# Performance work log

Hardware: AMD Instinct MI355X
Metric: run time of the kernel (lower is better)

Reference implementation:

```python
import jax, jax.numpy as jnp
import numpy as np

E, I, O = 8, 1024, 1024   # num_experts, in_features, out_features
B = 16                    # number of molecular systems (segments)
N = 16384                 # total rows (atoms * coeffs); sum(mole_sizes) == N


def setup_inputs() -> dict:
    key = jax.random.key(0)
    k1, k2, k3, k4 = jax.random.split(key, 4)
    scale = (1.0 / I) ** 0.5
    x = jax.random.normal(k1, (N, I), dtype=jnp.float32)
    # init_linear: uniform(-k, k) with k = sqrt(1/in_features)
    weights = scale * 2.0 * (jax.random.uniform(k2, (E, O, I), dtype=jnp.float32) - 0.5)
    bias = scale * 2.0 * (jax.random.uniform(k3, (O,), dtype=jnp.float32) - 0.5)
    expert_mixing_coefficients = jax.random.uniform(k4, (B, E), dtype=jnp.float32)
    # segment sizes per system; equal sizes summing exactly to N (static under jit)
    mole_sizes = jnp.full((B,), N // B, dtype=jnp.int32)
    return {
        "x": x,
        "weights": weights,
        "bias": bias,
        "expert_mixing_coefficients": expert_mixing_coefficients,
        "mole_sizes": mole_sizes,
    }


def reference(x, weights, bias, expert_mixing_coefficients, mole_sizes):
    # Original: W_b = einsum('eoi,be->bio', weights, coeff); then segment_mm
    # applies x_seg_b @ W_b for each row-segment b.  By linearity this equals
    # projecting x through each expert and mixing with per-row coefficients,
    # which avoids materializing [B, I, O] synthesized weights per segment
    # while computing identical math.
    n = x.shape[0]
    b = expert_mixing_coefficients.shape[0]
    seg_id = jnp.repeat(jnp.arange(b), mole_sizes, total_repeat_length=n)  # [N]
    ct = expert_mixing_coefficients[seg_id]                               # [N, E]
    proj = jnp.einsum('ni,eoi->neo', x, weights)                          # [N, E, O]
    y = jnp.einsum('neo,ne->no', proj, ct) + bias                         # [N, O]
    return y
```

## Files before the change

### kernel.cpp

```cpp
#include <hip/hip_runtime.h>
#include <hip/hip_bf16.h>
#include <stdint.h>

constexpr int E_NUM  = 8;
constexpr int I_DIM  = 1024;
constexpr int O_DIM  = 1024;
constexpr int B_SEG  = 16;
constexpr int N_ROWS = 16384;

constexpr int BM = 256, BN = 256, BK = 64;
constexpr int NT = I_DIM / BK;

typedef __bf16 bf16x8 __attribute__((ext_vector_type(8)));
typedef float  f32x4  __attribute__((ext_vector_type(4)));
typedef unsigned short ushortx4 __attribute__((ext_vector_type(4)));

#define AS1 __attribute__((address_space(1)))
#define AS3 __attribute__((address_space(3)))

__device__ __forceinline__ unsigned short f2bf(float f) {
    unsigned int u = __float_as_uint(f);
    u += 0x7fffu + ((u >> 16) & 1u);
    return (unsigned short)(u >> 16);
}

__global__ __launch_bounds__(256) void prep(const float* __restrict__ x,
                                            unsigned short* __restrict__ xb,
                                            const float* __restrict__ w,
                                            const float* __restrict__ coeff,
                                            unsigned short* __restrict__ wb) {
    __shared__ float sc[B_SEG * E_NUM];
    const int bid = blockIdx.x;
    const int tid = threadIdx.x;
    const int q  = bid / 5;
    const int r5 = bid % 5;

    if (r5 == 0) {
        if (tid < B_SEG * E_NUM) sc[tid] = coeff[tid];
        __syncthreads();

        const size_t idx = ((size_t)q * 256 + tid) * 4;
        float4 wv[E_NUM];
#pragma unroll
        for (int e = 0; e < E_NUM; e++)
            wv[e] = *(const float4*)(w + (size_t)e * O_DIM * I_DIM + idx);

#pragma unroll
        for (int b = 0; b < B_SEG; b++) {
            float a0 = 0.f, a1 = 0.f, a2 = 0.f, a3 = 0.f;
#pragma unroll
            for (int e = 0; e < E_NUM; e++) {
                const float c = sc[b * E_NUM + e];
                a0 += c * wv[e].x; a1 += c * wv[e].y;
                a2 += c * wv[e].z; a3 += c * wv[e].w;
            }
            ushortx4 o;
            o[0] = f2bf(a0); o[1] = f2bf(a1); o[2] = f2bf(a2); o[3] = f2bf(a3);
            *(ushortx4*)(wb + (size_t)b * O_DIM * I_DIM + idx) = o;
        }
    } else {
        const int cidx = q * 4 + (r5 - 1);
        const size_t base = (size_t)cidx * 4096;
#pragma unroll
        for (int k = 0; k < 4; k++) {
            const size_t i = base + (size_t)(k * 256 + tid) * 4;
            const float4 v = *(const float4*)(x + i);
            ushortx4 o;
            o[0] = f2bf(v.x); o[1] = f2bf(v.y); o[2] = f2bf(v.z); o[3] = f2bf(v.w);
            *(ushortx4*)(xb + i) = o;
        }
    }
}

__device__ __forceinline__ bf16x8 lds_read_b128(unsigned addr) {
    bf16x8 r;
    asm volatile("ds_read_b128 %0, %1" : "=v"(r) : "v"(addr));
    return r;
}

__global__ __launch_bounds__(512, 2) void gemm_moe(
    const unsigned short* __restrict__ xb,
    const unsigned short* __restrict__ wb,
    const float* __restrict__ bias,
    const int* __restrict__ msz,
    float* __restrict__ out)
{
    __shared__ __align__(16) char sLDS[131072];

    const int lid  = blockIdx.x;
    const int xcd  = lid & 7;
    const int idx  = lid >> 3;
    const int seg  = (xcd << 1) | (idx >> 4);
    const int t16  = idx & 15;
    const int mblk = t16 >> 2;
    const int nblk = t16 & 3;

    int off = 0;
    for (int b = 0; b < seg; b++) off += msz[b];
    const int row0 = off + mblk * BM;
    const int col0 = nblk * BN;
    const unsigned short* wseg = wb + (size_t)seg * O_DIM * I_DIM;

    const int tid  = threadIdx.x;
    const int wave = tid >> 6;
    const int lane = tid & 63;
    const int wr = wave >> 2, wc = wave & 3;
    const int quad = lane >> 4, l16 = lane & 15;

    const int srow8  = lane >> 3;
    const int schunk = (lane & 7) ^ srow8;
    const unsigned short* gA0 = xb   + (size_t)(row0 + wave * 8 + srow8) * I_DIM + schunk * 8;
    const unsigned short* gA1 = gA0 + (size_t)128 * I_DIM;
    const unsigned short* gB0 = wseg + (size_t)(col0 + wave * 8 + srow8) * I_DIM + schunk * 8;
    const unsigned short* gB1 = gB0 + (size_t)128 * I_DIM;

    const unsigned rdA0 = (unsigned)((wr * 16 + l16) * 128 + (((0 + quad) ^ (l16 & 7)) * 16));
    const unsigned rdA1 = (unsigned)((wr * 16 + l16) * 128 + (((4 + quad) ^ (l16 & 7)) * 16));
    const unsigned rdB0 = (unsigned)(65536 + (wc * 16 + l16) * 128 + (((0 + quad) ^ (l16 & 7)) * 16));
    const unsigned rdB1 = (unsigned)(65536 + (wc * 16 + l16) * 128 + (((4 + quad) ^ (l16 & 7)) * 16));

    bf16x8 af0[4][2], af1[4][2], b0[2][2], b1[2][2];
    f32x4 acc[8][4];
#pragma unroll
    for (int m = 0; m < 8; ++m)
#pragma unroll
        for (int n = 0; n < 4; ++n)
            acc[m][n] = (f32x4){0.f, 0.f, 0.f, 0.f};

#define LOAD_A(DST, S) do { _Pragma("unroll") for (int mm = 0; mm < 4; ++mm) {      \
        DST[mm][0] = lds_read_b128(rdA0 + (S) * 16384u + mm * 4096u);               \
        DST[mm][1] = lds_read_b128(rdA1 + (S) * 16384u + mm * 4096u); } } while (0)
#define LOAD_B(DST, S) do { _Pragma("unroll") for (int nn = 0; nn < 2; ++nn) {      \
        DST[nn][0] = lds_read_b128(rdB0 + (S) * 16384u + nn * 8192u);               \
        DST[nn][1] = lds_read_b128(rdB1 + (S) * 16384u + nn * 8192u); } } while (0)

#define STAGE_A(H, S, ST) do {                                                      \
        const unsigned short* g_ = ((H) ? gA1 : gA0) + (size_t)(ST) * 64;           \
        __builtin_amdgcn_global_load_lds((const AS1 void*)g_,                       \
            (AS3 void*)(sLDS + (S) * 16384 + wave * 1024), 16, 0, 0);               \
        __builtin_amdgcn_global_load_lds((const AS1 void*)(g_ + (size_t)64 * I_DIM),\
            (AS3 void*)(sLDS + (S) * 16384 + 8192 + wave * 1024), 16, 0, 0); } while (0)
#define STAGE_B(H, S, ST) do {                                                      \
        const unsigned short* g_ = ((H) ? gB1 : gB0) + (size_t)(ST) * 64;           \
        __builtin_amdgcn_global_load_lds((const AS1 void*)g_,                       \
            (AS3 void*)(sLDS + 65536 + (S) * 16384 + wave * 1024), 16, 0, 0);       \
        __builtin_amdgcn_global_load_lds((const AS1 void*)(g_ + (size_t)64 * I_DIM),\
            (AS3 void*)(sLDS + 65536 + (S) * 16384 + 8192 + wave * 1024), 16, 0, 0); } while (0)

#define MFMA_Q(MH, NH, A, BV) do { _Pragma("unroll") for (int mm = 0; mm < 4; ++mm) \
        _Pragma("unroll") for (int nn = 0; nn < 2; ++nn)                            \
        _Pragma("unroll") for (int kk = 0; kk < 2; ++kk)                            \
            acc[(MH) * 4 + mm][(NH) * 2 + nn] =                                     \
                __builtin_amdgcn_mfma_f32_16x16x32_bf16(A[mm][kk], BV[nn][kk],      \
                    acc[(MH) * 4 + mm][(NH) * 2 + nn], 0, 0, 0); } while (0)

#define PH_MID() do { __builtin_amdgcn_sched_barrier(0);                            \
        __builtin_amdgcn_s_barrier();                                               \
        asm volatile("s_waitcnt lgkmcnt(0)");                                       \
        __builtin_amdgcn_sched_barrier(0);                                          \
        __builtin_amdgcn_s_setprio(1); } while (0)
#define PH_END_W() do { __builtin_amdgcn_s_setprio(0);                              \
        __builtin_amdgcn_sched_barrier(0);                                          \
        asm volatile("s_waitcnt vmcnt(4)");                                         \
        __builtin_amdgcn_sched_barrier(0);                                          \
        __builtin_amdgcn_s_barrier(); } while (0)
#define PH_END_N() do { __builtin_amdgcn_s_setprio(0);                              \
        __builtin_amdgcn_sched_barrier(0);                                          \
        __builtin_amdgcn_s_barrier(); } while (0)

#define TILE(R0, R1, S0, S1, ST) do {                                               \
        LOAD_A(af0, R0); LOAD_B(b0, R0); STAGE_A(0, S0, ST);                        \
        PH_MID(); MFMA_Q(0, 0, af0, b0); PH_END_W();                                \
        LOAD_A(af1, R1); STAGE_B(0, S0, ST);                                        \
        PH_MID(); MFMA_Q(1, 0, af1, b0); PH_END_W();                                \
        LOAD_B(b1, R1); STAGE_A(1, S1, ST);                                         \
        PH_MID(); MFMA_Q(1, 1, af1, b1); PH_END_N();                                \
        STAGE_B(1, S1, ST);                                                         \
        PH_MID(); MFMA_Q(0, 1, af0, b1); PH_END_W();                                \
    } while (0)

    STAGE_A(0, 0, 0); STAGE_B(0, 0, 0);
    STAGE_A(1, 1, 0); STAGE_B(1, 1, 0);
    asm volatile("s_waitcnt vmcnt(4)");
    __builtin_amdgcn_sched_barrier(0);
    __builtin_amdgcn_s_barrier();

#pragma unroll 1
    for (int tp = 0; tp < 8; ++tp) {
        const int t0 = 2 * tp, t1 = t0 + 1;
        const int st0 = (t0 + 1 < NT) ? t0 + 1 : NT - 1;
        const int st1 = (t1 + 1 < NT) ? t1 + 1 : NT - 1;
        TILE(0, 1, 2, 3, st0);
        TILE(2, 3, 0, 1, st1);
    }

#undef TILE
#undef PH_END_N
#undef PH_END_W
#undef PH_MID
#undef MFMA_Q
#undef STAGE_B
#undef STAGE_A
#undef LOAD_B
#undef LOAD_A

    float bv[4];
#pragma unroll
    for (int n = 0; n < 4; ++n)
        bv[n] = bias[col0 + n * 64 + wc * 16 + l16];

#pragma unroll
    for (int m = 0; m < 8; ++m) {
#pragma unroll
        for (int r = 0; r < 4; ++r) {
            int row = row0 + m * 32 + wr * 16 + quad * 4 + r;
            float* po = out + (size_t)row * O_DIM + col0 + wc * 16 + l16;
#pragma unroll
            for (int n = 0; n < 4; ++n)
                po[n * 64] = acc[m][n][r] + bv[n];
        }
    }
}

extern "C" void kernel_launch(void* const* d_in, const int* in_sizes, int n_in,
                              void* d_out, int out_size, void* d_ws, size_t ws_size,
                              hipStream_t stream) {
    const float* x     = (const float*)d_in[0];
    const float* w     = (const float*)d_in[1];
    const float* bias  = (const float*)d_in[2];
    const float* coeff = (const float*)d_in[3];
    const int*   msz   = (const int*)d_in[4];
    float* out = (float*)d_out;

    unsigned short* xb = (unsigned short*)d_ws;
    unsigned short* wb = xb + (size_t)N_ROWS * I_DIM;

    prep<<<5120, 256, 0, stream>>>(x, xb, w, coeff, wb);

    gemm_moe<<<B_SEG * (1024 / BM) * (1024 / BN), 512, 0, stream>>>(xb, wb, bias, msz, out);
}
```

Baseline: 195.4 us.

## Fuse x fp32-to-bf16 conversion into GEMM A-tile staging via registers

Drops the separate pass that converted x to bf16 in the prep kernel. The GEMM now loads fp32 x rows into registers, packs them to bf16 with v_cvt_pk_bf16_f32, and writes them swizzled into LDS inside the pipelined tile loop. The prep kernel now only synthesizes the mixed weights, with each thread handling two vectors. This removes the 64MB fp32 read plus 32MB bf16 write and read round trip for x. In exchange each GEMM tile reads x at twice the bytes, uses more registers, and adds LDS write traffic and tighter wait scheduling. Within the 4x4 tile grid of each segment, the four N-blocks sharing an M-block each load and convert the same x rows.

Measured after the change: 203.2 us. 4.0% more time.

```diff
diff --git a/kernel.cpp b/kernel.cpp
--- a/kernel.cpp
+++ b/kernel.cpp
@@ -14,6 +14,7 @@
 typedef __bf16 bf16x8 __attribute__((ext_vector_type(8)));
 typedef float  f32x4  __attribute__((ext_vector_type(4)));
 typedef unsigned short ushortx4 __attribute__((ext_vector_type(4)));
+typedef unsigned int   u32x4    __attribute__((ext_vector_type(4)));
 
 #define AS1 __attribute__((address_space(1)))
 #define AS3 __attribute__((address_space(3)))
@@ -24,51 +25,40 @@
     return (unsigned short)(u >> 16);
 }
 
-__global__ __launch_bounds__(256) void prep(const float* __restrict__ x,
-                                            unsigned short* __restrict__ xb,
-                                            const float* __restrict__ w,
+__global__ __launch_bounds__(256) void prep(const float* __restrict__ w,
                                             const float* __restrict__ coeff,
                                             unsigned short* __restrict__ wb) {
     __shared__ float sc[B_SEG * E_NUM];
-    const int bid = blockIdx.x;
     const int tid = threadIdx.x;
-    const int q  = bid / 5;
-    const int r5 = bid % 5;
-
-    if (r5 == 0) {
-        if (tid < B_SEG * E_NUM) sc[tid] = coeff[tid];
-        __syncthreads();
-
-        const size_t idx = ((size_t)q * 256 + tid) * 4;
-        float4 wv[E_NUM];
-#pragma unroll
-        for (int e = 0; e < E_NUM; e++)
-            wv[e] = *(const float4*)(w + (size_t)e * O_DIM * I_DIM + idx);
-
-#pragma unroll
-        for (int b = 0; b < B_SEG; b++) {
-            float a0 = 0.f, a1 = 0.f, a2 = 0.f, a3 = 0.f;
-#pragma unroll
-            for (int e = 0; e < E_NUM; e++) {
-                const float c = sc[b * E_NUM + e];
-                a0 += c * wv[e].x; a1 += c * wv[e].y;
-                a2 += c * wv[e].z; a3 += c * wv[e].w;
-            }
-            ushortx4 o;
-            o[0] = f2bf(a0); o[1] = f2bf(a1); o[2] = f2bf(a2); o[3] = f2bf(a3);
-            *(ushortx4*)(wb + (size_t)b * O_DIM * I_DIM + idx) = o;
+    if (tid < B_SEG * E_NUM) sc[tid] = coeff[tid];
+    __syncthreads();
+
+    const size_t s0 = (size_t)blockIdx.x * 512 + tid;
+    const size_t s1 = s0 + 256;
+    float4 wv0[E_NUM], wv1[E_NUM];
+#pragma unroll
+    for (int e = 0; e < E_NUM; e++) {
+        wv0[e] = *(const float4*)(w + (size_t)e * O_DIM * I_DIM + s0 * 4);
+        wv1[e] = *(const float4*)(w + (size_t)e * O_DIM * I_DIM + s1 * 4);
+    }
+
+#pragma unroll
+    for (int b = 0; b < B_SEG; b++) {
+        float a0 = 0.f, a1 = 0.f, a2 = 0.f, a3 = 0.f;
+        float c0 = 0.f, c1 = 0.f, c2 = 0.f, c3 = 0.f;
+#pragma unroll
+        for (int e = 0; e < E_NUM; e++) {
+            const float c = sc[b * E_NUM + e];
+            a0 += c * wv0[e].x; a1 += c * wv0[e].y;
+            a2 += c * wv0[e].z; a3 += c * wv0[e].w;
+            c0 += c * wv1[e].x; c1 += c * wv1[e].y;
+            c2 += c * wv1[e].z; c3 += c * wv1[e].w;
         }
-    } else {
-        const int cidx = q * 4 + (r5 - 1);
-        const size_t base = (size_t)cidx * 4096;
-#pragma unroll
-        for (int k = 0; k < 4; k++) {
-            const size_t i = base + (size_t)(k * 256 + tid) * 4;
-            const float4 v = *(const float4*)(x + i);
-            ushortx4 o;
-            o[0] = f2bf(v.x); o[1] = f2bf(v.y); o[2] = f2bf(v.z); o[3] = f2bf(v.w);
-            *(ushortx4*)(xb + i) = o;
-        }
+        ushortx4 o0, o1;
+        o0[0] = f2bf(a0); o0[1] = f2bf(a1); o0[2] = f2bf(a2); o0[3] = f2bf(a3);
+        o1[0] = f2bf(c0); o1[1] = f2bf(c1); o1[2] = f2bf(c2); o1[3] = f2bf(c3);
+        *(ushortx4*)(wb + (size_t)b * O_DIM * I_DIM + s0 * 4) = o0;
+        *(ushortx4*)(wb + (size_t)b * O_DIM * I_DIM + s1 * 4) = o1;
     }
 }
 
@@ -77,9 +67,17 @@
     asm volatile("ds_read_b128 %0, %1" : "=v"(r) : "v"(addr));
     return r;
 }
+__device__ __forceinline__ void lds_write_b128(unsigned addr, u32x4 v) {
+    asm volatile("ds_write_b128 %0, %1" :: "v"(addr), "v"(v) : "memory");
+}
+__device__ __forceinline__ unsigned cvt_pk_bf16(float lo, float hi) {
+    unsigned r;
+    asm("v_cvt_pk_bf16_f32 %0, %1, %2" : "=v"(r) : "v"(lo), "v"(hi));
+    return r;
+}
 
 __global__ __launch_bounds__(512, 2) void gemm_moe(
-    const unsigned short* __restrict__ xb,
+    const float* __restrict__ x,
     const unsigned short* __restrict__ wb,
     const float* __restrict__ bias,
     const int* __restrict__ msz,
@@ -109,10 +107,15 @@
 
     const int srow8  = lane >> 3;
     const int schunk = (lane & 7) ^ srow8;
-    const unsigned short* gA0 = xb   + (size_t)(row0 + wave * 8 + srow8) * I_DIM + schunk * 8;
-    const unsigned short* gA1 = gA0 + (size_t)128 * I_DIM;
     const unsigned short* gB0 = wseg + (size_t)(col0 + wave * 8 + srow8) * I_DIM + schunk * 8;
     const unsigned short* gB1 = gB0 + (size_t)128 * I_DIM;
+
+    const int arow   = tid >> 2;
+    const int acpair = tid & 3;
+    const float* xA = x + (size_t)(row0 + arow) * I_DIM + acpair * 16;
+    const unsigned awr = (unsigned)(arow * 128);
+    const unsigned aw0 = (unsigned)(((2 * acpair)     ^ (arow & 7)) * 16);
+    const unsigned aw1 = (unsigned)(((2 * acpair + 1) ^ (arow & 7)) * 16);
 
     const unsigned rdA0 = (unsigned)((wr * 16 + l16) * 128 + (((0 + quad) ^ (l16 & 7)) * 16));
     const unsigned rdA1 = (unsigned)((wr * 16 + l16) * 128 + (((4 + quad) ^ (l16 & 7)) * 16));
@@ -120,6 +123,8 @@
     const unsigned rdB1 = (unsigned)(65536 + (wc * 16 + l16) * 128 + (((4 + quad) ^ (l16 & 7)) * 16));
 
     bf16x8 af0[4][2], af1[4][2], b0[2][2], b1[2][2];
+    float4 rA0_0, rA0_1, rA0_2, rA0_3;
+    float4 rA1_0, rA1_1, rA1_2, rA1_3;
     f32x4 acc[8][4];
 #pragma unroll
     for (int m = 0; m < 8; ++m)
@@ -134,12 +139,22 @@
         DST[nn][0] = lds_read_b128(rdB0 + (S) * 16384u + nn * 8192u);               \
         DST[nn][1] = lds_read_b128(rdB1 + (S) * 16384u + nn * 8192u); } } while (0)
 
-#define STAGE_A(H, S, ST) do {                                                      \
-        const unsigned short* g_ = ((H) ? gA1 : gA0) + (size_t)(ST) * 64;           \
-        __builtin_amdgcn_global_load_lds((const AS1 void*)g_,                       \
-            (AS3 void*)(sLDS + (S) * 16384 + wave * 1024), 16, 0, 0);               \
-        __builtin_amdgcn_global_load_lds((const AS1 void*)(g_ + (size_t)64 * I_DIM),\
-            (AS3 void*)(sLDS + (S) * 16384 + 8192 + wave * 1024), 16, 0, 0); } while (0)
+#define A_ISSUE(P, H, ST) do {                                                      \
+        const float* g_ = xA + (size_t)(H) * 128 * I_DIM + (ST) * 64;               \
+        P##_0 = *(const float4*)(g_);                                               \
+        P##_1 = *(const float4*)(g_ + 4);                                           \
+        P##_2 = *(const float4*)(g_ + 8);                                           \
+        P##_3 = *(const float4*)(g_ + 12); } while (0)
+
+#define A_WRITE(P, S) do {                                                          \
+        u32x4 u0_, u1_;                                                             \
+        u0_[0] = cvt_pk_bf16(P##_0.x, P##_0.y); u0_[1] = cvt_pk_bf16(P##_0.z, P##_0.w); \
+        u0_[2] = cvt_pk_bf16(P##_1.x, P##_1.y); u0_[3] = cvt_pk_bf16(P##_1.z, P##_1.w); \
+        u1_[0] = cvt_pk_bf16(P##_2.x, P##_2.y); u1_[1] = cvt_pk_bf16(P##_2.z, P##_2.w); \
+        u1_[2] = cvt_pk_bf16(P##_3.x, P##_3.y); u1_[3] = cvt_pk_bf16(P##_3.z, P##_3.w); \
+        lds_write_b128((S) * 16384u + awr + aw0, u0_);                              \
+        lds_write_b128((S) * 16384u + awr + aw1, u1_); } while (0)
+
 #define STAGE_B(H, S, ST) do {                                                      \
         const unsigned short* g_ = ((H) ? gB1 : gB0) + (size_t)(ST) * 64;           \
         __builtin_amdgcn_global_load_lds((const AS1 void*)g_,                       \
@@ -159,29 +174,44 @@
         asm volatile("s_waitcnt lgkmcnt(0)");                                       \
         __builtin_amdgcn_sched_barrier(0);                                          \
         __builtin_amdgcn_s_setprio(1); } while (0)
-#define PH_END_W() do { __builtin_amdgcn_s_setprio(0);                              \
+
+#define TILE(R0, R1, S0, S1, ST) do {                                               \
+                                     \
+        A_ISSUE(rA0, 0, ST);                                                        \
+        LOAD_A(af0, R0); LOAD_B(b0, R0);                                            \
+        PH_MID(); MFMA_Q(0, 0, af0, b0);                                            \
+        __builtin_amdgcn_s_setprio(0); __builtin_amdgcn_sched_barrier(0);           \
+        asm volatile("s_waitcnt vmcnt(4)");                \
+        __builtin_amdgcn_sched_barrier(0); __builtin_amdgcn_s_barrier();            \
+                                           \
+        LOAD_A(af1, R1); STAGE_B(0, S0, ST);                                        \
+        PH_MID(); MFMA_Q(1, 0, af1, b0);                                            \
+        __builtin_amdgcn_s_setprio(0); __builtin_amdgcn_sched_barrier(0);           \
+        __builtin_amdgcn_s_barrier();                                               \
+                  \
+        LOAD_B(b1, R1); A_ISSUE(rA1, 1, ST);                                        \
+        PH_MID(); MFMA_Q(1, 1, af1, b1);                                            \
+        __builtin_amdgcn_s_setprio(0); __builtin_amdgcn_sched_barrier(0);           \
+        A_WRITE(rA0, S0);                             \
+        __builtin_amdgcn_sched_barrier(0); __builtin_amdgcn_s_barrier();            \
+                        \
+        STAGE_B(1, S1, ST);                                                         \
+        PH_MID(); MFMA_Q(0, 1, af0, b1);                                            \
+        __builtin_amdgcn_s_setprio(0); __builtin_amdgcn_sched_barrier(0);           \
+        asm volatile("s_waitcnt vmcnt(2)");                    \
         __builtin_amdgcn_sched_barrier(0);                                          \
-        asm volatile("s_waitcnt vmcnt(4)");                                         \
-        __builtin_amdgcn_sched_barrier(0);                                          \
-        __builtin_amdgcn_s_barrier(); } while (0)
-#define PH_END_N() do { __builtin_amdgcn_s_setprio(0);                              \
-        __builtin_amdgcn_sched_barrier(0);                                          \
-        __builtin_amdgcn_s_barrier(); } while (0)
-
-#define TILE(R0, R1, S0, S1, ST) do {                                               \
-        LOAD_A(af0, R0); LOAD_B(b0, R0); STAGE_A(0, S0, ST);                        \
-        PH_MID(); MFMA_Q(0, 0, af0, b0); PH_END_W();                                \
-        LOAD_A(af1, R1); STAGE_B(0, S0, ST);                                        \
-        PH_MID(); MFMA_Q(1, 0, af1, b0); PH_END_W();                                \
-        LOAD_B(b1, R1); STAGE_A(1, S1, ST);                                         \
-        PH_MID(); MFMA_Q(1, 1, af1, b1); PH_END_N();                                \
-        STAGE_B(1, S1, ST);                                                         \
-        PH_MID(); MFMA_Q(0, 1, af0, b1); PH_END_W();                                \
+        A_WRITE(rA1, S1);                                                           \
+        asm volatile("s_waitcnt lgkmcnt(0)");             \
+        __builtin_amdgcn_sched_barrier(0); __builtin_amdgcn_s_barrier();            \
     } while (0)
 
-    STAGE_A(0, 0, 0); STAGE_B(0, 0, 0);
-    STAGE_A(1, 1, 0); STAGE_B(1, 1, 0);
-    asm volatile("s_waitcnt vmcnt(4)");
+    A_ISSUE(rA0, 0, 0);
+    A_ISSUE(rA1, 1, 0);
+    STAGE_B(0, 0, 0);
+    STAGE_B(1, 1, 0);
+    A_WRITE(rA0, 0);
+    A_WRITE(rA1, 1);
+    asm volatile("s_waitcnt vmcnt(0) lgkmcnt(0)");
     __builtin_amdgcn_sched_barrier(0);
     __builtin_amdgcn_s_barrier();
 
@@ -193,14 +223,14 @@
         TILE(0, 1, 2, 3, st0);
         TILE(2, 3, 0, 1, st1);
     }
+    asm volatile("s_waitcnt vmcnt(0) lgkmcnt(0)");
 
 #undef TILE
-#undef PH_END_N
-#undef PH_END_W
 #undef PH_MID
 #undef MFMA_Q
 #undef STAGE_B
-#undef STAGE_A
+#undef A_WRITE
+#undef A_ISSUE
 #undef LOAD_B
 #undef LOAD_A
 
@@ -232,10 +262,9 @@
     const int*   msz   = (const int*)d_in[4];
     float* out = (float*)d_out;
 
-    unsigned short* xb = (unsigned short*)d_ws;
-    unsigned short* wb = xb + (size_t)N_ROWS * I_DIM;
-
-    prep<<<5120, 256, 0, stream>>>(x, xb, w, coeff, wb);
-
-    gemm_moe<<<B_SEG * (1024 / BM) * (1024 / BN), 512, 0, stream>>>(xb, wb, bias, msz, out);
-}
+    unsigned short* wb = (unsigned short*)d_ws;
+
+    prep<<<512, 256, 0, stream>>>(w, coeff, wb);
+
+    gemm_moe<<<B_SEG * (1024 / BM) * (1024 / BN), 512, 0, stream>>>(x, wb, bias, msz, out);
+}
```
